# Kernel optimization log

Hardware: AMD Instinct MI355X
Metric: run time of the kernel (lower is better)

The kernel has to match this reference:

```python
import jax, jax.numpy as jnp
import numpy as np

D_MODEL = 1024
N_HEAD = 16
DH = D_MODEL // N_HEAD


def setup_inputs() -> dict:
    key = jax.random.key(0)
    ks = jax.random.split(key, 5)
    B, T = 4, 2048
    scale = 0.02
    return {
        "x": jax.random.normal(ks[0], (B, T, D_MODEL), dtype=jnp.float32),
        "Wqkv": jax.random.normal(ks[1], (D_MODEL, 3 * D_MODEL), dtype=jnp.float32) * scale,
        "bqkv": jnp.zeros((3 * D_MODEL,), dtype=jnp.float32),
        "Wout": jax.random.normal(ks[2], (D_MODEL, D_MODEL), dtype=jnp.float32) * scale,
        "bout": jnp.zeros((D_MODEL,), dtype=jnp.float32),
    }


def reference(x, Wqkv, bqkv, Wout, bout):
    B, T, C = x.shape
    qkv = x @ Wqkv + bqkv  # [B,T,3C]
    q, k, v = jnp.split(qkv, 3, axis=2)
    # [B,T,C] -> [B,H,T,dh]
    def heads(t):
        return t.reshape(B, T, N_HEAD, DH).transpose(0, 2, 1, 3)
    q, k, v = heads(q), heads(k), heads(v)
    scores = jnp.einsum("bhqd,bhkd->bhqk", q, k) / jnp.sqrt(jnp.float32(DH))
    causal = jnp.tril(jnp.ones((T, T), dtype=bool))  # [T,T]
    neg = jnp.finfo(scores.dtype).min
    scores = jnp.where(causal[None, None, :, :], scores, neg)
    A = jax.nn.softmax(scores, axis=-1)
    y = jnp.einsum("bhqk,bhkd->bhqd", A, v)
    y = y.transpose(0, 2, 1, 3).reshape(B, T, C)
    return y @ Wout + bout
```

## Files before the change

### kernel.cpp

```cpp
#include <hip/hip_runtime.h>
#include <hip/hip_bf16.h>

typedef float f32x4 __attribute__((ext_vector_type(4)));
typedef float f32x16 __attribute__((ext_vector_type(16)));
typedef short s16x8 __attribute__((ext_vector_type(8)));
typedef short s16x4 __attribute__((ext_vector_type(4)));
typedef unsigned int u32x4 __attribute__((ext_vector_type(4)));

#define B_ 4
#define T_ 2048
#define C_ 1024
#define H_ 16
#define DH_ 64
#define M_ (B_*T_)
#define N3_ (3*C_)

static __device__ __forceinline__ short f2bf(float f) {
    __hip_bfloat16 h = __float2bfloat16(f);
    return *reinterpret_cast<short*>(&h);
}

static __device__ __forceinline__ unsigned pack2(float lo, float hi) {
    unsigned r;
    asm("v_cvt_pk_bf16_f32 %0, %1, %2" : "=v"(r) : "v"(lo), "v"(hi));
    return r;
}

static __device__ __forceinline__ float exp2_raw(float x) {
    float r;
    asm("v_exp_f32 %0, %1" : "=v"(r) : "v"(x));
    return r;
}

static __device__ __forceinline__ void gload16(const void* g, void* l) {
    __builtin_amdgcn_global_load_lds(
        (const __attribute__((address_space(1))) void*)g,
        (__attribute__((address_space(3))) void*)l, 16, 0, 0);
}

static __device__ __forceinline__ s16x8 lds_frag(const short* base, int row, int chunk) {
    return *(const s16x8*)&base[(row << 6) + ((chunk ^ (row & 7)) << 3)];
}


__global__ __launch_bounds__(256) void cast_f32_bf16(
    const float* __restrict__ in, short* __restrict__ out, int n8)
{
    int i = blockIdx.x * 256 + threadIdx.x;
    if (i >= n8) return;
    float4 a = *(const float4*)&in[i * 8];
    float4 b = *(const float4*)&in[i * 8 + 4];
    s16x8 o = { f2bf(a.x), f2bf(a.y), f2bf(a.z), f2bf(a.w),
                f2bf(b.x), f2bf(b.y), f2bf(b.z), f2bf(b.w) };
    *(s16x8*)&out[i * 8] = o;
}

__global__ __launch_bounds__(256) void transpose_cast(
    const float* __restrict__ src, short* __restrict__ dst, int K, int N)
{
    __shared__ short t[64][66];
    int tid = threadIdx.x;
    int n0 = blockIdx.x * 64, k0 = blockIdx.y * 64;
    #pragma unroll
    for (int p = 0; p < 4; ++p) {
        int cid = tid + p * 256;
        int r = cid >> 4, c4 = cid & 15;
        float4 v = *(const float4*)&src[(size_t)(k0 + r) * N + n0 + c4 * 4];
        t[r][c4 * 4 + 0] = f2bf(v.x);
        t[r][c4 * 4 + 1] = f2bf(v.y);
        t[r][c4 * 4 + 2] = f2bf(v.z);
        t[r][c4 * 4 + 3] = f2bf(v.w);
    }
    __syncthreads();
    #pragma unroll
    for (int p = 0; p < 4; ++p) {
        int cid = tid + p * 256;
        int r = cid >> 4, c4 = cid & 15;
        s16x4 ov;
        #pragma unroll
        for (int j = 0; j < 4; ++j) ov[j] = t[c4 * 4 + j][r];
        *(s16x4*)&dst[(size_t)(n0 + r) * K + k0 + c4 * 4] = ov;
    }
}


template<int MODE>
__global__ __launch_bounds__(256) void gemm_bt(
    const short* __restrict__ A, const short* __restrict__ Bt,
    const float* __restrict__ bias, float* __restrict__ out,
    short* __restrict__ qout, short* __restrict__ kout, short* __restrict__ vout)
{
    const int K = 1024;
    __shared__ short As[2][128 * 64];
    __shared__ short Bs[2][128 * 64];
    int tid = threadIdx.x;
    int lane = tid & 63, w = tid >> 6;
    int d = lane & 15, g = lane >> 4;
    int wm = w >> 1, wn = w & 1;

    int gx = gridDim.x;
    int lid = blockIdx.y * gx + blockIdx.x;
    int chunk = (gx * gridDim.y) >> 3;
    int sl = (lid & 7) * chunk + (lid >> 3);
    int m0 = (sl / gx) * 128, n0 = (sl % gx) * 128;

    f32x4 acc[4][4];
    #pragma unroll
    for (int i = 0; i < 4; ++i)
        #pragma unroll
        for (int j = 0; j < 4; ++j) acc[i][j] = (f32x4){0.f, 0.f, 0.f, 0.f};

    int r_ = tid >> 3, c8_ = tid & 7;
    int co_ = (c8_ ^ (r_ & 7)) << 3;

    #define GSTAGE(buf, kt) do { \
        _Pragma("unroll") \
        for (int p = 0; p < 4; ++p) { \
            int rr = p * 32 + r_; \
            int dofs = (p * 256 + (tid & ~63)) * 8; \
            gload16(&A[(size_t)(m0 + rr) * K + (kt) + co_], &As[buf][dofs]); \
            gload16(&Bt[(size_t)(n0 + rr) * K + (kt) + co_], &Bs[buf][dofs]); \
        } \
    } while (0)

    GSTAGE(0, 0);
    int cur = 0;

    #pragma unroll 1
    for (int kt = 0; kt < K; kt += 64) {
        if (kt + 64 < K) {
            GSTAGE(cur ^ 1, kt + 64);
            asm volatile("s_waitcnt vmcnt(8)" ::: "memory");
        } else {
            asm volatile("s_waitcnt vmcnt(0)" ::: "memory");
        }
        __builtin_amdgcn_s_barrier();

        const short* Ab = As[cur];
        const short* Bb = Bs[cur];
        #pragma unroll
        for (int ks = 0; ks < 2; ++ks) {
            s16x8 af[4], bf[4];
            #pragma unroll
            for (int i = 0; i < 4; ++i) {
                af[i] = lds_frag(Ab, wm * 64 + i * 16 + d, ks * 4 + g);
                bf[i] = lds_frag(Bb, wn * 64 + i * 16 + d, ks * 4 + g);
            }
            #pragma unroll
            for (int mi = 0; mi < 4; ++mi)
                #pragma unroll
                for (int ni = 0; ni < 4; ++ni)
                    acc[mi][ni] = __builtin_amdgcn_mfma_f32_16x16x32_bf16(
                        af[mi], bf[ni], acc[mi][ni], 0, 0, 0);
        }

        __builtin_amdgcn_s_barrier();
        cur ^= 1;
    }
    #undef GSTAGE

    #pragma unroll
    for (int mi = 0; mi < 4; ++mi)
        #pragma unroll
        for (int ni = 0; ni < 4; ++ni) {
            int gn = n0 + wn * 64 + ni * 16 + d;
            float bv = bias[gn];
            int gm0 = m0 + wm * 64 + mi * 16 + g * 4;
            if (MODE == 0) {
                #pragma unroll
                for (int r = 0; r < 4; ++r)
                    out[(size_t)(gm0 + r) * 1024 + gn] = acc[mi][ni][r] + bv;
            } else {
                int which = gn >> 10, cc = gn & 1023;
                int h = cc >> 6, dh = cc & 63;
                int b = gm0 >> 11;
                if (which == 2) {
                    int g2 = ((g & 1) << 1) | (g >> 1);
                    int t0v = (gm0 & 2047) - g * 4 + g2 * 4;
                    s16x4 pv;
                    #pragma unroll
                    for (int r = 0; r < 4; ++r) pv[r] = f2bf(acc[mi][ni][r] + bv);
                    *(s16x4*)&vout[((size_t)(b * 16 + h) * 64 + dh) * 2048 + t0v] = pv;
                } else if (which == 1) {
                    int t0 = gm0 & 2047;
                    #pragma unroll
                    for (int r = 0; r < 4; ++r)
                        kout[((size_t)(b * 16 + h) * 2048 + (t0 + r)) * 64 + dh] =
                            f2bf(acc[mi][ni][r] + bv);
                } else {
                    int t0 = gm0 & 2047;
                    const float SC2 = 0.125f * 1.44269504089f;
                    #pragma unroll
                    for (int r = 0; r < 4; ++r)
                        qout[((size_t)(b * 16 + h) * 2048 + (t0 + r)) * 64 + dh] =
                            f2bf((acc[mi][ni][r] + bv) * SC2);
                }
            }
        }
}


__global__ __launch_bounds__(256, 4) void attn_fwd(
    const short* __restrict__ q, const short* __restrict__ kk,
    const short* __restrict__ vt, short* __restrict__ y)
{
    __shared__ short Ks[2][64 * 64];
    __shared__ short Vs[2][64 * 64];
    int tid = threadIdx.x, w = tid >> 6;
    int lane = tid & 63;
    int q5 = lane & 31, h5 = lane >> 5;
    int bid = blockIdx.x;
    int idx = bid >> 3;
    int qt = 15 - (idx >> 3);
    int bh = ((idx & 7) << 3) | (bid & 7);
    int b = bh >> 4, hh = bh & 15;
    const size_t hb = (size_t)bh * 2048 * 64;
    int nt = 2 * qt + 2;
    int qrow = qt * 128 + w * 32;
    int qg = qrow + q5;

    s16x8 qf[4];
    #pragma unroll
    for (int s = 0; s < 4; ++s)
        qf[s] = *(const s16x8*)&q[hb + (size_t)qg * 64 + 16 * s + 8 * h5];

    f32x16 oA, oB;
    #pragma unroll
    for (int i = 0; i < 16; ++i) { oA[i] = 0.f; oB[i] = 0.f; }
    float l = 0.f;

    #define STAGE(buf, kt2) do { \
        _Pragma("unroll") \
        for (int p = 0; p < 2; ++p) { \
            int cid = p * 256 + tid; \
            int r__ = cid >> 3, c8__ = cid & 7; \
            int co__ = (c8__ ^ (r__ & 7)) << 3; \
            int dofs__ = (p * 256 + (tid & ~63)) * 8; \
            gload16(&kk[hb + (size_t)((kt2) * 64 + r__) * 64 + co__], &Ks[buf][dofs__]); \
            gload16(&vt[hb + (size_t)r__ * 2048 + (kt2) * 64 + co__], &Vs[buf][dofs__]); \
        } \
    } while (0)

    STAGE(0, 0);
    int cur = 0;

    #pragma unroll 1
    for (int t = 0; t < nt; ++t) {
        if (t + 1 < nt) {
            STAGE(cur ^ 1, t + 1);
            asm volatile("s_waitcnt vmcnt(4)" ::: "memory");
        } else {
            asm volatile("s_waitcnt vmcnt(0)" ::: "memory");
        }
        __builtin_amdgcn_s_barrier();

        if (t * 64 <= qrow + 31) {
            const short* Kb = Ks[cur];
            const short* Vb = Vs[cur];

            f32x16 sA, sB;
            #pragma unroll
            for (int i = 0; i < 16; ++i) { sA[i] = 0.f; sB[i] = 0.f; }
            #pragma unroll
            for (int s = 0; s < 4; ++s) {
                sA = __builtin_amdgcn_mfma_f32_32x32x16_bf16(
                    lds_frag(Kb, q5, 2 * s + h5), qf[s], sA, 0, 0, 0);
                sB = __builtin_amdgcn_mfma_f32_32x32x16_bf16(
                    lds_frag(Kb, 32 + q5, 2 * s + h5), qf[s], sB, 0, 0, 0);
            }

            float eA[16], eB[16];
            float S = 0.f;
            if (t * 64 + 63 > qrow) {
                #pragma unroll
                for (int rg = 0; rg < 16; ++rg) {
                    int kg = t * 64 + (rg & 3) + 8 * (rg >> 2) + 4 * h5;
                    float a = exp2_raw(sA[rg]); if (kg > qg) a = 0.f;
                    float c = exp2_raw(sB[rg]); if (kg + 32 > qg) c = 0.f;
                    eA[rg] = a; eB[rg] = c; S += a + c;
                }
            } else {
                #pragma unroll
                for (int rg = 0; rg < 16; ++rg) {
                    float a = exp2_raw(sA[rg]);
                    float c = exp2_raw(sB[rg]);
                    eA[rg] = a; eB[rg] = c; S += a + c;
                }
            }
            l += S;

            unsigned wdA[8], wdB[8];
            #pragma unroll
            for (int m = 0; m < 4; ++m) {
                wdA[2 * m]     = pack2(eA[4 * m],     eA[4 * m + 1]);
                wdA[2 * m + 1] = pack2(eA[4 * m + 2], eA[4 * m + 3]);
                wdB[2 * m]     = pack2(eB[4 * m],     eB[4 * m + 1]);
                wdB[2 * m + 1] = pack2(eB[4 * m + 2], eB[4 * m + 3]);
            }

            #pragma unroll
            for (int kc = 0; kc < 4; ++kc) {
                const unsigned* wsrc = (kc < 2) ? wdA : wdB;
                int o4 = (kc & 1) << 2;
                u32x4 pw = {wsrc[o4], wsrc[o4 + 1], wsrc[o4 + 2], wsrc[o4 + 3]};
                s16x8 pb = __builtin_bit_cast(s16x8, pw);
                oA = __builtin_amdgcn_mfma_f32_32x32x16_bf16(
                    lds_frag(Vb, q5, 2 * kc + h5), pb, oA, 0, 0, 0);
                oB = __builtin_amdgcn_mfma_f32_32x32x16_bf16(
                    lds_frag(Vb, 32 + q5, 2 * kc + h5), pb, oB, 0, 0, 0);
            }
        }

        __builtin_amdgcn_s_barrier();
        cur ^= 1;
    }

    l += __shfl_xor(l, 32);
    float rl = 1.0f / l;

    short* yp = &y[(size_t)(b * 2048 + qg) * 1024 + hh * 64];
    #pragma unroll
    for (int m = 0; m < 4; ++m) {
        s16x4 v0, v1;
        #pragma unroll
        for (int i = 0; i < 4; ++i) {
            v0[i] = f2bf(oA[4 * m + i] * rl);
            v1[i] = f2bf(oB[4 * m + i] * rl);
        }
        *(s16x4*)&yp[8 * m + 4 * h5] = v0;
        *(s16x4*)&yp[32 + 8 * m + 4 * h5] = v1;
    }
    #undef STAGE
}


extern "C" void kernel_launch(void* const* d_in, const int* in_sizes, int n_in,
                              void* d_out, int out_size, void* d_ws, size_t ws_size,
                              hipStream_t stream)
{
    const float* x    = (const float*)d_in[0];
    const float* Wqkv = (const float*)d_in[1];
    const float* bqkv = (const float*)d_in[2];
    const float* Wout = (const float*)d_in[3];
    const float* bout = (const float*)d_in[4];
    float* out = (float*)d_out;

    char* ws = (char*)d_ws;
    short* xbf   = (short*)ws;  ws += (size_t)M_ * C_ * 2;
    short* wqkvT = (short*)ws;  ws += (size_t)N3_ * C_ * 2;
    short* woutT = (short*)ws;  ws += (size_t)C_ * C_ * 2;
    short* qb    = (short*)ws;  ws += (size_t)M_ * C_ * 2;
    short* kb    = (short*)ws;  ws += (size_t)M_ * C_ * 2;
    short* vtb   = (short*)ws;  ws += (size_t)M_ * C_ * 2;
    short* yb    = (short*)ws;  ws += (size_t)M_ * C_ * 2;

    cast_f32_bf16<<<(M_ * C_ / 8 + 255) / 256, 256, 0, stream>>>(x, xbf, M_ * C_ / 8);
    transpose_cast<<<dim3(N3_ / 64, C_ / 64), 256, 0, stream>>>(Wqkv, wqkvT, C_, N3_);
    transpose_cast<<<dim3(C_ / 64, C_ / 64), 256, 0, stream>>>(Wout, woutT, C_, C_);

    gemm_bt<1><<<dim3(N3_ / 128, M_ / 128), 256, 0, stream>>>(
        xbf, wqkvT, bqkv, nullptr, qb, kb, vtb);

    attn_fwd<<<dim3((T_ / 128) * B_ * H_), 256, 0, stream>>>(qb, kb, vtb, yb);

    gemm_bt<0><<<dim3(C_ / 128, M_ / 128), 256, 0, stream>>>(
        yb, woutT, bout, out, nullptr, nullptr, nullptr);
}
```

Baseline: 171.2 us.

## Pair complementary causal query tiles in one 512-thread attention block sharing K/V staging

```diff
diff --git a/kernel.cpp b/kernel.cpp
--- a/kernel.cpp
+++ b/kernel.cpp
@@ -200,7 +200,7 @@
 }
 
 
-__global__ __launch_bounds__(256, 4) void attn_fwd(
+__global__ __launch_bounds__(512, 4) void attn_fwd(
     const short* __restrict__ q, const short* __restrict__ kk,
     const short* __restrict__ vt, short* __restrict__ y)
 {
@@ -210,14 +210,26 @@
     int lane = tid & 63;
     int q5 = lane & 31, h5 = lane >> 5;
     int bid = blockIdx.x;
-    int idx = bid >> 3;
-    int qt = 15 - (idx >> 3);
-    int bh = ((idx & 7) << 3) | (bid & 7);
-    int b = bh >> 4, hh = bh & 15;
-    const size_t hb = (size_t)bh * 2048 * 64;
-    int nt = 2 * qt + 2;
-    int qrow = qt * 128 + w * 32;
+    int stripe = bid & 7;
+    int pi = (bid >> 3) & 7;
+    int hi = bid >> 6;
+    int head = hi * 8 + stripe;
+    int b = head >> 4, hh = head & 15;
+    const size_t hb = (size_t)head * 2048 * 64;
+    int qt = (w >> 2) ? pi : (15 - pi);
+    int wl = w & 3;
+    int nt = 2 * (15 - pi) + 2;
+    int qrow = qt * 128 + wl * 32;
     int qg = qrow + q5;
+
+    int r_ = tid >> 3, c8_ = tid & 7;
+    int co_ = (c8_ ^ (r_ & 7)) << 3;
+    int dofs_ = (tid & ~63) * 8;
+
+    #define STAGE(buf, kt2) do { \
+        gload16(&kk[hb + (size_t)((kt2) * 64 + r_) * 64 + co_], &Ks[buf][dofs_]); \
+        gload16(&vt[hb + (size_t)r_ * 2048 + (kt2) * 64 + co_], &Vs[buf][dofs_]); \
+    } while (0)
 
     s16x8 qf[4];
     #pragma unroll
@@ -228,18 +240,6 @@
     #pragma unroll
     for (int i = 0; i < 16; ++i) { oA[i] = 0.f; oB[i] = 0.f; }
     float l = 0.f;
-
-    #define STAGE(buf, kt2) do { \
-        _Pragma("unroll") \
-        for (int p = 0; p < 2; ++p) { \
-            int cid = p * 256 + tid; \
-            int r__ = cid >> 3, c8__ = cid & 7; \
-            int co__ = (c8__ ^ (r__ & 7)) << 3; \
-            int dofs__ = (p * 256 + (tid & ~63)) * 8; \
-            gload16(&kk[hb + (size_t)((kt2) * 64 + r__) * 64 + co__], &Ks[buf][dofs__]); \
-            gload16(&vt[hb + (size_t)r__ * 2048 + (kt2) * 64 + co__], &Vs[buf][dofs__]); \
-        } \
-    } while (0)
 
     STAGE(0, 0);
     int cur = 0;
@@ -248,7 +248,7 @@
     for (int t = 0; t < nt; ++t) {
         if (t + 1 < nt) {
             STAGE(cur ^ 1, t + 1);
-            asm volatile("s_waitcnt vmcnt(4)" ::: "memory");
+            asm volatile("s_waitcnt vmcnt(2)" ::: "memory");
         } else {
             asm volatile("s_waitcnt vmcnt(0)" ::: "memory");
         }
@@ -260,7 +260,7 @@
 
             f32x16 sA, sB;
             #pragma unroll
-            for (int i = 0; i < 16; ++i) { sA[i] = 0.f; sB[i] = 0.f; }
+            for (int i2 = 0; i2 < 16; ++i2) { sA[i2] = 0.f; sB[i2] = 0.f; }
             #pragma unroll
             for (int s = 0; s < 4; ++s) {
                 sA = __builtin_amdgcn_mfma_f32_32x32x16_bf16(
@@ -361,7 +361,7 @@
     gemm_bt<1><<<dim3(N3_ / 128, M_ / 128), 256, 0, stream>>>(
         xbf, wqkvT, bqkv, nullptr, qb, kb, vtb);
 
-    attn_fwd<<<dim3((T_ / 128) * B_ * H_), 256, 0, stream>>>(qb, kb, vtb, yb);
+    attn_fwd<<<dim3(512), 512, 0, stream>>>(qb, kb, vtb, yb);
 
     gemm_bt<0><<<dim3(C_ / 128, M_ / 128), 256, 0, stream>>>(
         yb, woutT, bout, out, nullptr, nullptr, nullptr);
```

Result: no change. 174.0 us (+1.7%).

## Defer PV matmul to next iteration to overlap with K/V staging

Applied to the files above, without the earlier changes.

```diff
diff --git a/kernel.cpp b/kernel.cpp
--- a/kernel.cpp
+++ b/kernel.cpp
@@ -229,6 +229,9 @@
     for (int i = 0; i < 16; ++i) { oA[i] = 0.f; oB[i] = 0.f; }
     float l = 0.f;
 
+    unsigned wdA[8], wdB[8];
+    bool haveP = false;
+
     #define STAGE(buf, kt2) do { \
         _Pragma("unroll") \
         for (int p = 0; p < 2; ++p) { \
@@ -241,11 +244,30 @@
         } \
     } while (0)
 
+    #define PV_STEP(Vb) do { \
+        _Pragma("unroll") \
+        for (int kc = 0; kc < 4; ++kc) { \
+            const unsigned* wsrc = (kc < 2) ? wdA : wdB; \
+            int o4 = (kc & 1) << 2; \
+            u32x4 pw = {wsrc[o4], wsrc[o4 + 1], wsrc[o4 + 2], wsrc[o4 + 3]}; \
+            s16x8 pb = __builtin_bit_cast(s16x8, pw); \
+            oA = __builtin_amdgcn_mfma_f32_32x32x16_bf16( \
+                lds_frag((Vb), q5, 2 * kc + h5), pb, oA, 0, 0, 0); \
+            oB = __builtin_amdgcn_mfma_f32_32x32x16_bf16( \
+                lds_frag((Vb), 32 + q5, 2 * kc + h5), pb, oB, 0, 0, 0); \
+        } \
+    } while (0)
+
     STAGE(0, 0);
     int cur = 0;
 
     #pragma unroll 1
     for (int t = 0; t < nt; ++t) {
+        if (haveP) {
+            PV_STEP(Vs[cur ^ 1]);
+        }
+        __builtin_amdgcn_s_barrier();
+
         if (t + 1 < nt) {
             STAGE(cur ^ 1, t + 1);
             asm volatile("s_waitcnt vmcnt(4)" ::: "memory");
@@ -256,11 +278,10 @@
 
         if (t * 64 <= qrow + 31) {
             const short* Kb = Ks[cur];
-            const short* Vb = Vs[cur];
 
             f32x16 sA, sB;
             #pragma unroll
-            for (int i = 0; i < 16; ++i) { sA[i] = 0.f; sB[i] = 0.f; }
+            for (int i2 = 0; i2 < 16; ++i2) { sA[i2] = 0.f; sB[i2] = 0.f; }
             #pragma unroll
             for (int s = 0; s < 4; ++s) {
                 sA = __builtin_amdgcn_mfma_f32_32x32x16_bf16(
@@ -289,7 +310,6 @@
             }
             l += S;
 
-            unsigned wdA[8], wdB[8];
             #pragma unroll
             for (int m = 0; m < 4; ++m) {
                 wdA[2 * m]     = pack2(eA[4 * m],     eA[4 * m + 1]);
@@ -297,22 +317,16 @@
                 wdB[2 * m]     = pack2(eB[4 * m],     eB[4 * m + 1]);
                 wdB[2 * m + 1] = pack2(eB[4 * m + 2], eB[4 * m + 3]);
             }
-
-            #pragma unroll
-            for (int kc = 0; kc < 4; ++kc) {
-                const unsigned* wsrc = (kc < 2) ? wdA : wdB;
-                int o4 = (kc & 1) << 2;
-                u32x4 pw = {wsrc[o4], wsrc[o4 + 1], wsrc[o4 + 2], wsrc[o4 + 3]};
-                s16x8 pb = __builtin_bit_cast(s16x8, pw);
-                oA = __builtin_amdgcn_mfma_f32_32x32x16_bf16(
-                    lds_frag(Vb, q5, 2 * kc + h5), pb, oA, 0, 0, 0);
-                oB = __builtin_amdgcn_mfma_f32_32x32x16_bf16(
-                    lds_frag(Vb, 32 + q5, 2 * kc + h5), pb, oB, 0, 0, 0);
-            }
-        }
-
-        __builtin_amdgcn_s_barrier();
+            haveP = true;
+        } else {
+            haveP = false;
+        }
+
         cur ^= 1;
+    }
+
+    if (haveP) {
+        PV_STEP(Vs[cur ^ 1]);
     }
 
     l += __shfl_xor(l, 32);
@@ -331,6 +345,7 @@
         *(s16x4*)&yp[32 + 8 * m + 4 * h5] = v1;
     }
     #undef STAGE
+    #undef PV_STEP
 }
 
 
```

After: 171.5 us. No clear change (+0.2%).
